# Kernel tuning notes

Hardware: AMD Instinct MI355X
Metric: run time of the kernel (lower is better)

The kernel has to match this reference:

```python
import jax, jax.numpy as jnp
import numpy as np

NPOINT = 512
NSAMPLE = 32
RADIUS = 0.2


def furthest_point_sampling(pts, npoint):
    # pts: (B, N, 3) -> (B, npoint) int32 indices
    B, N, _ = pts.shape

    def step(carry, _):
        dist, far = carry  # (B,N), (B,)
        centroid = jnp.take_along_axis(pts, far[:, None, None], axis=1)  # (B,1,3)
        d2 = jnp.sum((pts - centroid) ** 2, axis=-1)  # (B,N)
        dist = jnp.minimum(dist, d2)
        nfar = jnp.argmax(dist, axis=-1).astype(jnp.int32)
        return (dist, nfar), far

    init = (jnp.full((B, N), 1e10, pts.dtype), jnp.zeros((B,), jnp.int32))
    _, idxs = jax.lax.scan(step, init, None, length=npoint)
    return idxs.T  # (B, npoint)


def ball_query(new_xyz, xyz, nsample, radius):
    # new_xyz: (B,S,3), xyz: (B,N,3) -> (B,S,nsample) int32
    N = xyz.shape[1]
    d2 = jnp.sum((new_xyz[:, :, None, :] - xyz[:, None, :, :]) ** 2, axis=-1)  # (B,S,N)
    ar = jnp.arange(N, dtype=jnp.int32)
    key = jnp.where(d2 < radius * radius, ar, N)  # valid idx, else sentinel N
    idx = jnp.sort(key, axis=-1)[..., :nsample]  # first nsample in-radius indices
    first = idx[..., :1]
    idx = jnp.where(idx == N, first, idx)  # pad with first valid (CUDA ball_query behavior)
    return jnp.minimum(idx, N - 1)


def group_points(feat, idx):
    # feat: (B,C,N), idx: (B,S,K) -> (B,C,S,K)
    return jax.vmap(lambda f, i: f[:, i])(feat, idx)


def pointnet_sa(xyz, features, W1, b1, W2, b2, W3, b3):
    xyz_t = jnp.transpose(xyz, (0, 2, 1))  # (B,N,3)
    fps_idx = furthest_point_sampling(xyz_t, NPOINT)  # (B,S)
    new_xyz = group_points(xyz, fps_idx[:, :, None])[..., 0]  # (B,3,S)
    idx = ball_query(jnp.transpose(new_xyz, (0, 2, 1)), xyz_t, NSAMPLE, RADIUS)  # (B,S,K)
    grouped_xyz = group_points(xyz, idx) - new_xyz[:, :, :, None]  # (B,3,S,K), centered
    grouped_feat = group_points(features, idx)  # (B,C,S,K)
    h = jnp.concatenate([grouped_xyz, grouped_feat], axis=1)  # (B,C+3,S,K)
    for W, b in ((W1, b1), (W2, b2), (W3, b3)):
        h = jax.nn.relu(jnp.einsum('oc,bcsk->bosk', W, h) + b[None, :, None, None])
    new_features = jnp.max(h, axis=3)  # (B,out,S)
    return new_xyz, new_features


def setup_inputs() -> dict:
    key = jax.random.key(0)
    ks = jax.random.split(key, 8)
    B, N, C = 16, 2048, 64
    return {
        'xyz': jax.random.uniform(ks[0], (B, 3, N), dtype=jnp.float32),
        'features': jax.random.normal(ks[1], (B, C, N), dtype=jnp.float32),
        'W1': jax.random.normal(ks[2], (64, 67), dtype=jnp.float32) * 0.1,
        'b1': jnp.zeros((64,), jnp.float32),
        'W2': jax.random.normal(ks[3], (128, 64), dtype=jnp.float32) * 0.1,
        'b2': jnp.zeros((128,), jnp.float32),
        'W3': jax.random.normal(ks[4], (256, 128), dtype=jnp.float32) * 0.1,
        'b3': jnp.zeros((256,), jnp.float32),
    }


def reference(xyz, features, W1, b1, W2, b2, W3, b3):
    return pointnet_sa(xyz, features, W1, b1, W2, b2, W3, b3)
```

## Files before the change

kernel.cpp:

```cpp
#include <hip/hip_runtime.h>

#define NB 16
#define NN 2048
#define NP 512
#define NS 32
#define NC 64

typedef _Float16 f16x8 __attribute__((ext_vector_type(8)));
typedef _Float16 f16x4 __attribute__((ext_vector_type(4)));
typedef float f32x4 __attribute__((ext_vector_type(4)));
typedef float f32x2 __attribute__((ext_vector_type(2)));

__device__ __forceinline__ float sqdist(float dx, float dy, float dz) {
  return __fadd_rn(__fadd_rn(__fmul_rn(dx, dx), __fmul_rn(dy, dy)), __fmul_rn(dz, dz));
}

__device__ __forceinline__ f32x2 pk_add(f32x2 a, f32x2 b) {
  f32x2 d;
  asm("v_pk_add_f32 %0, %1, %2" : "=v"(d) : "v"(a), "v"(b));
  return d;
}
__device__ __forceinline__ f32x2 pk_mul(f32x2 a, f32x2 b) {
  f32x2 d;
  asm("v_pk_mul_f32 %0, %1, %2" : "=v"(d) : "v"(a), "v"(b));
  return d;
}

template <int CTRL>
__device__ __forceinline__ float dppmaxf(float m) {
  int t = __builtin_amdgcn_update_dpp(0, __float_as_int(m), CTRL, 0xf, 0xf, true);
  return fmaxf(m, __int_as_float(t));
}
template <int CTRL>
__device__ __forceinline__ unsigned dppmaxu(unsigned m) {
  int t = __builtin_amdgcn_update_dpp(0, (int)m, CTRL, 0xf, 0xf, true);
  return m > (unsigned)t ? m : (unsigned)t;
}

__global__ __launch_bounds__(256) void prep_kernel(const float* __restrict__ feat,
                                                   const float* __restrict__ xyz,
                                                   _Float16* __restrict__ featF,
                                                   float* __restrict__ xyzT) {
  __shared__ float tile[64][65];
  const int b = blockIdx.x;
  const int n0 = blockIdx.y * 64;
  const int t = threadIdx.x;
  const int g = t >> 6, l = t & 63;
  if (g == 0) {
    int n = n0 + l;
    float4 q;
    q.x = xyz[(size_t)b * 3 * NN + n];
    q.y = xyz[(size_t)b * 3 * NN + NN + n];
    q.z = xyz[(size_t)b * 3 * NN + 2 * NN + n];
    q.w = 0.f;
    ((float4*)xyzT)[(size_t)b * NN + n] = q;
  }
#pragma unroll
  for (int r = 0; r < 16; ++r) {
    int c = g * 16 + r;
    tile[c][l] = feat[((size_t)b * NC + c) * NN + n0 + l];
  }
  __syncthreads();
#pragma unroll
  for (int r = 0; r < 16; ++r) {
    int nl = g * 16 + r;
    featF[((size_t)(b * NN + n0 + nl)) * NC + l] = (_Float16)tile[l][nl];
  }
}

__global__ __launch_bounds__(256) void wconv_kernel(const float* __restrict__ W1,
                                                    const float* __restrict__ W2,
                                                    const float* __restrict__ W3,
                                                    _Float16* __restrict__ W1f,
                                                    _Float16* __restrict__ W2f,
                                                    _Float16* __restrict__ W3f) {
  int i = blockIdx.x * 256 + threadIdx.x;
  if (i < 64 * 96) {
    int o = i / 96, k = i - o * 96;
    float v = (k < 64) ? W1[o * 67 + 3 + k] : ((k < 67) ? W1[o * 67 + (k - 64)] : 0.f);
    W1f[i] = (_Float16)v;
  }
  if (i < 128 * 64) W2f[i] = (_Float16)W2[i];
  if (i < 256 * 128) W3f[i] = (_Float16)W3[i];
}

__global__ __launch_bounds__(128, 1) void fps_kernel(const float* __restrict__ xyz,
                                                     float* __restrict__ newxyz) {
  const int b = blockIdx.x, t = threadIdx.x;
  const int w = t >> 6;
  const float* X = xyz + (size_t)b * 3 * NN;
  __shared__ __align__(16) float4 XL[NN];
  __shared__ float cst[3][NP];
  __shared__ __align__(16) uint2 pairx[2][2];
  f32x2 px[8], py[8], pz[8], dist[8];
#pragma unroll
  for (int jj = 0; jj < 8; ++jj) {
    int n0 = t + 256 * jj, n1 = n0 + 128;
    px[jj] = f32x2{X[n0], X[n1]};
    py[jj] = f32x2{X[NN + n0], X[NN + n1]};
    pz[jj] = f32x2{X[2 * NN + n0], X[2 * NN + n1]};
    dist[jj] = f32x2{1e10f, 1e10f};
    XL[n0] = make_float4(px[jj].x, py[jj].x, pz[jj].x, 0.f);
    XL[n1] = make_float4(px[jj].y, py[jj].y, pz[jj].y, 0.f);
  }
  float cx = X[0], cy = X[NN], cz = X[2 * NN];
  const unsigned kb = 2047u - (unsigned)t;
  __syncthreads();
  int buf = 0;
  for (int i = 0; i < NP; ++i) {
    if (t == 0) {
      cst[0][i] = cx;
      cst[1][i] = cy;
      cst[2][i] = cz;
    }
    const f32x2 ncx = f32x2{-cx, -cx}, ncy = f32x2{-cy, -cy}, ncz = f32x2{-cz, -cz};
    float hm[8];
#pragma unroll
    for (int jj = 0; jj < 8; ++jj) {
      f32x2 dx = pk_add(px[jj], ncx);
      f32x2 dy = pk_add(py[jj], ncy);
      f32x2 dz = pk_add(pz[jj], ncz);
      f32x2 s = pk_add(pk_add(pk_mul(dx, dx), pk_mul(dy, dy)), pk_mul(dz, dz));
      f32x2 d = dist[jj];
      d.x = fminf(d.x, s.x);
      d.y = fminf(d.y, s.y);
      dist[jj] = d;
      hm[jj] = fmaxf(d.x, d.y);
    }
    float m = fmaxf(fmaxf(fmaxf(hm[0], hm[1]), fmaxf(hm[2], hm[3])),
                    fmaxf(fmaxf(hm[4], hm[5]), fmaxf(hm[6], hm[7])));
    m = dppmaxf<0x111>(m);
    m = dppmaxf<0x112>(m);
    m = dppmaxf<0x114>(m);
    m = dppmaxf<0x118>(m);
    m = dppmaxf<0x142>(m);
    m = dppmaxf<0x143>(m);
    const float vmax =
        __int_as_float(__builtin_amdgcn_readlane(__float_as_int(m), 63));
    unsigned jk = 0;
#pragma unroll
    for (int jj = 0; jj < 8; ++jj) {
      unsigned c0 = (dist[jj].x == vmax) ? (63u - 2u * jj) : 0u;
      unsigned c1 = (dist[jj].y == vmax) ? (63u - (2u * jj + 1u)) : 0u;
      unsigned c = c0 > c1 ? c0 : c1;
      jk = jk > c ? jk : c;
    }
    unsigned nk = (jk >= 48u) ? (kb - ((63u - jk) << 7)) : 0u;
    nk = dppmaxu<0x111>(nk);
    nk = dppmaxu<0x112>(nk);
    nk = dppmaxu<0x114>(nk);
    nk = dppmaxu<0x118>(nk);
    nk = dppmaxu<0x142>(nk);
    nk = dppmaxu<0x143>(nk);
    if ((t & 63) == 63) pairx[buf][w] = make_uint2(__float_as_uint(m), nk);
    __syncthreads();
    uint4 pr = *(const uint4*)&pairx[buf][0];
    bool take1 = (pr.z > pr.x) | ((pr.z == pr.x) & (pr.w > pr.y));
    unsigned ng = 2047u - (take1 ? pr.w : pr.y);
    float4 c = XL[ng];
    cx = c.x;
    cy = c.y;
    cz = c.z;
    buf ^= 1;
  }
  __syncthreads();
  for (int i = t; i < NP; i += 128) {
    newxyz[b * 3 * NP + i] = cst[0][i];
    newxyz[b * 3 * NP + NP + i] = cst[1][i];
    newxyz[b * 3 * NP + 2 * NP + i] = cst[2][i];
  }
}

__global__ __launch_bounds__(256) void ball_kernel(const float* __restrict__ xyz,
                                                   const float* __restrict__ newxyz,
                                                   int* __restrict__ idx) {
  const int b = blockIdx.x;
  const int s = blockIdx.y * 4 + (threadIdx.x >> 6);
  const int lane = threadIdx.x & 63;
  const float* X = xyz + (size_t)b * 3 * NN;
  const float cx = newxyz[b * 3 * NP + s];
  const float cy = newxyz[b * 3 * NP + NP + s];
  const float cz = newxyz[b * 3 * NP + 2 * NP + s];
  int* row = idx + ((size_t)(b * NP + s)) * NS;
  const float r2 = (float)(0.2 * 0.2);
  int total = 0, first = 0;
  bool havefirst = false;
  for (int c0 = 0; c0 < NN; c0 += 64) {
    int n = c0 + lane;
    float d2 = sqdist(X[n] - cx, X[NN + n] - cy, X[2 * NN + n] - cz);
    bool hit = d2 < r2;
    unsigned long long mask = __ballot(hit);
    if (!havefirst && mask) {
      first = c0 + __builtin_ctzll(mask);
      havefirst = true;
    }
    if (hit) {
      int pos = total + (int)__popcll(mask & ((1ull << lane) - 1ull));
      if (pos < NS) row[pos] = n;
    }
    total += (int)__popcll(mask);
    if (total >= NS) break;
  }
  if (total < NS && lane >= total && lane < NS) row[lane] = first;
}

#define HSTR 104
#define A1STR 72
#define A2STR 136
#define A1OFF 17408

__global__ __launch_bounds__(256) void mlp_kernel(
    const float* __restrict__ xyzT, const _Float16* __restrict__ featF,
    const int* __restrict__ idx, const float* __restrict__ newxyz,
    const _Float16* __restrict__ W1f, const float* __restrict__ b1,
    const _Float16* __restrict__ W2f, const float* __restrict__ b2,
    const _Float16* __restrict__ W3f, const float* __restrict__ b3, float* __restrict__ out) {
  __shared__ _Float16 smem[17408 + 9216];
  _Float16* hT = smem;
  _Float16* a1T = smem + A1OFF;
  const int b = blockIdx.x;
  const int s0 = blockIdx.y * 4;
  const int t = threadIdx.x;
  const int lane = t & 63, w = t >> 6;

  {
    const int col = t & 127, hf = t >> 7;
    const int s = s0 + (col >> 5), k = col & 31;
    const int n = idx[((size_t)(b * NP + s)) * NS + k];
    const _Float16* F = featF + (size_t)(b * NN + n) * NC;
#pragma unroll
    for (int j = 0; j < 4; ++j) {
      int p = hf * 4 + j;
      *(f16x8*)(&hT[col * HSTR + p * 8]) = *(const f16x8*)(F + p * 8);
    }
    if (hf == 0) {
      float4 pnt = ((const float4*)xyzT)[(size_t)b * NN + n];
      float cx = newxyz[b * 3 * NP + s];
      float cy = newxyz[b * 3 * NP + NP + s];
      float cz = newxyz[b * 3 * NP + 2 * NP + s];
      f16x8 v = {};
      v[0] = (_Float16)(pnt.x - cx);
      v[1] = (_Float16)(pnt.y - cy);
      v[2] = (_Float16)(pnt.z - cz);
      *(f16x8*)(&hT[col * HSTR + 64]) = v;
    } else {
      f16x8 z = {};
      *(f16x8*)(&hT[col * HSTR + 72]) = z;
      *(f16x8*)(&hT[col * HSTR + 80]) = z;
      *(f16x8*)(&hT[col * HSTR + 88]) = z;
    }
  }
  __syncthreads();

  const int cl = lane & 15;
  const int kg = lane >> 4;

  {
    f32x4 acc[8];
    {
      f32x4 bb = *(const f32x4*)(b1 + w * 16 + kg * 4);
#pragma unroll
      for (int ct = 0; ct < 8; ++ct) acc[ct] = bb;
    }
#pragma unroll
    for (int ks = 0; ks < 3; ++ks) {
      f16x8 A = *(const f16x8*)(W1f + (w * 16 + cl) * 96 + ks * 32 + kg * 8);
#pragma unroll
      for (int ct = 0; ct < 8; ++ct) {
        f16x8 B = *(const f16x8*)(&hT[(ct * 16 + cl) * HSTR + ks * 32 + kg * 8]);
        acc[ct] = __builtin_amdgcn_mfma_f32_16x16x32_f16(A, B, acc[ct], 0, 0, 0);
      }
    }
#pragma unroll
    for (int ct = 0; ct < 8; ++ct) {
      f16x4 v;
#pragma unroll
      for (int i2 = 0; i2 < 4; ++i2) v[i2] = (_Float16)fmaxf(acc[ct][i2], 0.f);
      *(f16x4*)(&a1T[(ct * 16 + cl) * A1STR + w * 16 + kg * 4]) = v;
    }
  }
  __syncthreads();

  {
    f32x4 acc[2][8];
#pragma unroll
    for (int r = 0; r < 2; ++r) {
      f32x4 bb = *(const f32x4*)(b2 + w * 32 + r * 16 + kg * 4);
#pragma unroll
      for (int ct = 0; ct < 8; ++ct) acc[r][ct] = bb;
    }
#pragma unroll
    for (int ks = 0; ks < 2; ++ks) {
      f16x8 A0 = *(const f16x8*)(W2f + (w * 32 + cl) * 64 + ks * 32 + kg * 8);
      f16x8 A1 = *(const f16x8*)(W2f + (w * 32 + 16 + cl) * 64 + ks * 32 + kg * 8);
#pragma unroll
      for (int ct = 0; ct < 8; ++ct) {
        f16x8 B = *(const f16x8*)(&a1T[(ct * 16 + cl) * A1STR + ks * 32 + kg * 8]);
        acc[0][ct] = __builtin_amdgcn_mfma_f32_16x16x32_f16(A0, B, acc[0][ct], 0, 0, 0);
        acc[1][ct] = __builtin_amdgcn_mfma_f32_16x16x32_f16(A1, B, acc[1][ct], 0, 0, 0);
      }
    }
#pragma unroll
    for (int r = 0; r < 2; ++r)
#pragma unroll
      for (int ct = 0; ct < 8; ++ct) {
        f16x4 v;
#pragma unroll
        for (int i2 = 0; i2 < 4; ++i2) v[i2] = (_Float16)fmaxf(acc[r][ct][i2], 0.f);
        *(f16x4*)(&hT[(ct * 16 + cl) * A2STR + w * 32 + r * 16 + kg * 4]) = v;
      }
  }
  __syncthreads();

  float* out2 = out + NB * 3 * NP;
#pragma unroll
  for (int rh = 0; rh < 2; ++rh) {
    f32x4 acc[2][8];
#pragma unroll
    for (int r = 0; r < 2; ++r) {
      f32x4 bb = *(const f32x4*)(b3 + w * 64 + rh * 32 + r * 16 + kg * 4);
#pragma unroll
      for (int ct = 0; ct < 8; ++ct) acc[r][ct] = bb;
    }
#pragma unroll
    for (int ks = 0; ks < 4; ++ks) {
      f16x8 A0 = *(const f16x8*)(W3f + (w * 64 + rh * 32 + cl) * 128 + ks * 32 + kg * 8);
      f16x8 A1 = *(const f16x8*)(W3f + (w * 64 + rh * 32 + 16 + cl) * 128 + ks * 32 + kg * 8);
#pragma unroll
      for (int ct = 0; ct < 8; ++ct) {
        f16x8 B = *(const f16x8*)(&hT[(ct * 16 + cl) * A2STR + ks * 32 + kg * 8]);
        acc[0][ct] = __builtin_amdgcn_mfma_f32_16x16x32_f16(A0, B, acc[0][ct], 0, 0, 0);
        acc[1][ct] = __builtin_amdgcn_mfma_f32_16x16x32_f16(A1, B, acc[1][ct], 0, 0, 0);
      }
    }
#pragma unroll
    for (int r = 0; r < 2; ++r)
#pragma unroll
      for (int sl = 0; sl < 4; ++sl) {
        float vv[4];
#pragma unroll
        for (int i2 = 0; i2 < 4; ++i2) {
          float m0 = fmaxf(acc[r][sl * 2][i2], 0.f);
          float m1 = fmaxf(acc[r][sl * 2 + 1][i2], 0.f);
          float mv = fmaxf(m0, m1);
          mv = fmaxf(mv, __shfl_xor(mv, 1, 64));
          mv = fmaxf(mv, __shfl_xor(mv, 2, 64));
          mv = fmaxf(mv, __shfl_xor(mv, 4, 64));
          mv = fmaxf(mv, __shfl_xor(mv, 8, 64));
          vv[i2] = mv;
        }
        if (cl == 0) {
          int ob = w * 64 + rh * 32 + r * 16 + kg * 4;
#pragma unroll
          for (int i2 = 0; i2 < 4; ++i2)
            out2[((size_t)(b * 256 + ob + i2)) * NP + s0 + sl] = vv[i2];
        }
      }
  }
}

extern "C" void kernel_launch(void* const* d_in, const int* in_sizes, int n_in, void* d_out,
                              int out_size, void* d_ws, size_t ws_size, hipStream_t stream) {
  const float* xyz = (const float*)d_in[0];
  const float* feat = (const float*)d_in[1];
  const float* W1 = (const float*)d_in[2];
  const float* b1 = (const float*)d_in[3];
  const float* W2 = (const float*)d_in[4];
  const float* b2 = (const float*)d_in[5];
  const float* W3 = (const float*)d_in[6];
  const float* b3 = (const float*)d_in[7];
  float* out = (float*)d_out;
  char* ws = (char*)d_ws;
  float* xyzT = (float*)ws;
  _Float16* featF = (_Float16*)(ws + 524288);
  int* idx = (int*)(ws + 4718592);
  _Float16* W1f = (_Float16*)(ws + 5767168);
  _Float16* W2f = (_Float16*)(ws + 5779456);
  _Float16* W3f = (_Float16*)(ws + 5795840);

  hipLaunchKernelGGL(prep_kernel, dim3(NB, 32), dim3(256), 0, stream, feat, xyz, featF, xyzT);
  hipLaunchKernelGGL(wconv_kernel, dim3(128), dim3(256), 0, stream, W1, W2, W3, W1f, W2f, W3f);
  hipLaunchKernelGGL(fps_kernel, dim3(NB), dim3(128), 0, stream, xyz, out);
  hipLaunchKernelGGL(ball_kernel, dim3(NB, 128), dim3(256), 0, stream, xyz, out, idx);
  hipLaunchKernelGGL(mlp_kernel, dim3(NB, 128), dim3(256), 0, stream, xyzT, featF, idx, out, W1f,
                     b1, W2f, b2, W3f, b3, out);
}
```

Baseline: 395.9 us.

## Merge prep, weight-convert and FPS into one kernel; widen FPS to 256 threads

Folds the feature transpose/convert, weight conversion and furthest point sampling into a single launch. Blocks 0-15 run FPS, blocks 16-527 do the prep tiles, and block 528 converts the weights, so the prep work overlaps the serial FPS. FPS now uses 256 threads with 8 points per thread instead of 16. The argmax-index search uses ballot plus count-trailing-zeros instead of a second DPP reduction. The trade-off is a 4-way cross-wave combine per iteration in place of 2-way, and the shared-memory footprint is shared with the prep path.

```diff
diff --git a/kernel.cpp b/kernel.cpp
--- a/kernel.cpp
+++ b/kernel.cpp
@@ -31,71 +31,68 @@
   int t = __builtin_amdgcn_update_dpp(0, __float_as_int(m), CTRL, 0xf, 0xf, true);
   return fmaxf(m, __int_as_float(t));
 }
-template <int CTRL>
-__device__ __forceinline__ unsigned dppmaxu(unsigned m) {
-  int t = __builtin_amdgcn_update_dpp(0, (int)m, CTRL, 0xf, 0xf, true);
-  return m > (unsigned)t ? m : (unsigned)t;
-}
-
-__global__ __launch_bounds__(256) void prep_kernel(const float* __restrict__ feat,
-                                                   const float* __restrict__ xyz,
-                                                   _Float16* __restrict__ featF,
-                                                   float* __restrict__ xyzT) {
-  __shared__ float tile[64][65];
-  const int b = blockIdx.x;
-  const int n0 = blockIdx.y * 64;
+
+__global__ __launch_bounds__(256, 1) void front_kernel(
+    const float* __restrict__ xyz, const float* __restrict__ feat,
+    const float* __restrict__ W1, const float* __restrict__ W2, const float* __restrict__ W3,
+    float* __restrict__ newxyz, _Float16* __restrict__ featF, float* __restrict__ xyzT,
+    _Float16* __restrict__ W1f, _Float16* __restrict__ W2f, _Float16* __restrict__ W3f) {
+  __shared__ __align__(16) char sm[39040];
+  const int bid = blockIdx.x;
   const int t = threadIdx.x;
-  const int g = t >> 6, l = t & 63;
-  if (g == 0) {
-    int n = n0 + l;
-    float4 q;
-    q.x = xyz[(size_t)b * 3 * NN + n];
-    q.y = xyz[(size_t)b * 3 * NN + NN + n];
-    q.z = xyz[(size_t)b * 3 * NN + 2 * NN + n];
-    q.w = 0.f;
-    ((float4*)xyzT)[(size_t)b * NN + n] = q;
-  }
-#pragma unroll
-  for (int r = 0; r < 16; ++r) {
-    int c = g * 16 + r;
-    tile[c][l] = feat[((size_t)b * NC + c) * NN + n0 + l];
-  }
-  __syncthreads();
-#pragma unroll
-  for (int r = 0; r < 16; ++r) {
-    int nl = g * 16 + r;
-    featF[((size_t)(b * NN + n0 + nl)) * NC + l] = (_Float16)tile[l][nl];
-  }
-}
-
-__global__ __launch_bounds__(256) void wconv_kernel(const float* __restrict__ W1,
-                                                    const float* __restrict__ W2,
-                                                    const float* __restrict__ W3,
-                                                    _Float16* __restrict__ W1f,
-                                                    _Float16* __restrict__ W2f,
-                                                    _Float16* __restrict__ W3f) {
-  int i = blockIdx.x * 256 + threadIdx.x;
-  if (i < 64 * 96) {
-    int o = i / 96, k = i - o * 96;
-    float v = (k < 64) ? W1[o * 67 + 3 + k] : ((k < 67) ? W1[o * 67 + (k - 64)] : 0.f);
-    W1f[i] = (_Float16)v;
-  }
-  if (i < 128 * 64) W2f[i] = (_Float16)W2[i];
-  if (i < 256 * 128) W3f[i] = (_Float16)W3[i];
-}
-
-__global__ __launch_bounds__(128, 1) void fps_kernel(const float* __restrict__ xyz,
-                                                     float* __restrict__ newxyz) {
-  const int b = blockIdx.x, t = threadIdx.x;
+
+  if (bid >= 16) {
+    if (bid == 528) {
+      for (int i = t; i < 256 * 128; i += 256) {
+        if (i < 64 * 96) {
+          int o = i / 96, k = i - o * 96;
+          float v = (k < 64) ? W1[o * 67 + 3 + k] : ((k < 67) ? W1[o * 67 + (k - 64)] : 0.f);
+          W1f[i] = (_Float16)v;
+        }
+        if (i < 128 * 64) W2f[i] = (_Float16)W2[i];
+        W3f[i] = (_Float16)W3[i];
+      }
+      return;
+    }
+    float(*tile)[65] = (float(*)[65])sm;
+    const int pb = bid - 16;
+    const int b = pb >> 5;
+    const int n0 = (pb & 31) * 64;
+    const int g = t >> 6, l = t & 63;
+    if (g == 0) {
+      int n = n0 + l;
+      float4 q;
+      q.x = xyz[(size_t)b * 3 * NN + n];
+      q.y = xyz[(size_t)b * 3 * NN + NN + n];
+      q.z = xyz[(size_t)b * 3 * NN + 2 * NN + n];
+      q.w = 0.f;
+      ((float4*)xyzT)[(size_t)b * NN + n] = q;
+    }
+#pragma unroll
+    for (int r = 0; r < 16; ++r) {
+      int c = g * 16 + r;
+      tile[c][l] = feat[((size_t)b * NC + c) * NN + n0 + l];
+    }
+    __syncthreads();
+#pragma unroll
+    for (int r = 0; r < 16; ++r) {
+      int nl = g * 16 + r;
+      featF[((size_t)(b * NN + n0 + nl)) * NC + l] = (_Float16)tile[l][nl];
+    }
+    return;
+  }
+
+  const int b = bid;
   const int w = t >> 6;
   const float* X = xyz + (size_t)b * 3 * NN;
-  __shared__ __align__(16) float4 XL[NN];
-  __shared__ float cst[3][NP];
-  __shared__ __align__(16) uint2 pairx[2][2];
-  f32x2 px[8], py[8], pz[8], dist[8];
-#pragma unroll
-  for (int jj = 0; jj < 8; ++jj) {
-    int n0 = t + 256 * jj, n1 = n0 + 128;
+  float4* XL = (float4*)sm;
+  float* cst = (float*)(sm + 32768);
+  uint2* ck = (uint2*)(sm + 32768 + 6144);
+
+  f32x2 px[4], py[4], pz[4], dist[4];
+#pragma unroll
+  for (int jj = 0; jj < 4; ++jj) {
+    int n0 = t + 256 * jj, n1 = n0 + 1024;
     px[jj] = f32x2{X[n0], X[n1]};
     py[jj] = f32x2{X[NN + n0], X[NN + n1]};
     pz[jj] = f32x2{X[2 * NN + n0], X[2 * NN + n1]};
@@ -104,19 +101,18 @@
     XL[n1] = make_float4(px[jj].y, py[jj].y, pz[jj].y, 0.f);
   }
   float cx = X[0], cy = X[NN], cz = X[2 * NN];
-  const unsigned kb = 2047u - (unsigned)t;
   __syncthreads();
   int buf = 0;
   for (int i = 0; i < NP; ++i) {
     if (t == 0) {
-      cst[0][i] = cx;
-      cst[1][i] = cy;
-      cst[2][i] = cz;
+      cst[i] = cx;
+      cst[NP + i] = cy;
+      cst[2 * NP + i] = cz;
     }
     const f32x2 ncx = f32x2{-cx, -cx}, ncy = f32x2{-cy, -cy}, ncz = f32x2{-cz, -cz};
-    float hm[8];
-#pragma unroll
-    for (int jj = 0; jj < 8; ++jj) {
+    float hm[4];
+#pragma unroll
+    for (int jj = 0; jj < 4; ++jj) {
       f32x2 dx = pk_add(px[jj], ncx);
       f32x2 dy = pk_add(py[jj], ncy);
       f32x2 dz = pk_add(pz[jj], ncz);
@@ -127,47 +123,43 @@
       dist[jj] = d;
       hm[jj] = fmaxf(d.x, d.y);
     }
-    float m = fmaxf(fmaxf(fmaxf(hm[0], hm[1]), fmaxf(hm[2], hm[3])),
-                    fmaxf(fmaxf(hm[4], hm[5]), fmaxf(hm[6], hm[7])));
+    float m = fmaxf(fmaxf(hm[0], hm[1]), fmaxf(hm[2], hm[3]));
     m = dppmaxf<0x111>(m);
     m = dppmaxf<0x112>(m);
     m = dppmaxf<0x114>(m);
     m = dppmaxf<0x118>(m);
     m = dppmaxf<0x142>(m);
     m = dppmaxf<0x143>(m);
-    const float vmax =
-        __int_as_float(__builtin_amdgcn_readlane(__float_as_int(m), 63));
-    unsigned jk = 0;
-#pragma unroll
-    for (int jj = 0; jj < 8; ++jj) {
-      unsigned c0 = (dist[jj].x == vmax) ? (63u - 2u * jj) : 0u;
-      unsigned c1 = (dist[jj].y == vmax) ? (63u - (2u * jj + 1u)) : 0u;
-      unsigned c = c0 > c1 ? c0 : c1;
-      jk = jk > c ? jk : c;
-    }
-    unsigned nk = (jk >= 48u) ? (kb - ((63u - jk) << 7)) : 0u;
-    nk = dppmaxu<0x111>(nk);
-    nk = dppmaxu<0x112>(nk);
-    nk = dppmaxu<0x114>(nk);
-    nk = dppmaxu<0x118>(nk);
-    nk = dppmaxu<0x142>(nk);
-    nk = dppmaxu<0x143>(nk);
-    if ((t & 63) == 63) pairx[buf][w] = make_uint2(__float_as_uint(m), nk);
+    const float vmax = __int_as_float(__builtin_amdgcn_readlane(__float_as_int(m), 63));
+    unsigned long long mm[8];
+#pragma unroll
+    for (int jj = 0; jj < 4; ++jj) {
+      mm[jj] = __ballot(dist[jj].x == vmax);
+      mm[4 + jj] = __ballot(dist[jj].y == vmax);
+    }
+    unsigned nw = 0;
+#pragma unroll
+    for (int q = 7; q >= 0; --q)
+      if (mm[q]) nw = 256u * (unsigned)q + (unsigned)(w << 6) + (unsigned)__builtin_ctzll(mm[q]);
+    if ((t & 63) == 0) ck[buf * 4 + w] = make_uint2(__float_as_uint(vmax), nw);
     __syncthreads();
-    uint4 pr = *(const uint4*)&pairx[buf][0];
-    bool take1 = (pr.z > pr.x) | ((pr.z == pr.x) & (pr.w > pr.y));
-    unsigned ng = 2047u - (take1 ? pr.w : pr.y);
-    float4 c = XL[ng];
+    uint4 c01 = *(const uint4*)&ck[buf * 4 + 0];
+    uint4 c23 = *(const uint4*)&ck[buf * 4 + 2];
+    unsigned v = c01.x, n = c01.y;
+    if (c01.z > v || (c01.z == v && c01.w < n)) { v = c01.z; n = c01.w; }
+    if (c23.x > v || (c23.x == v && c23.y < n)) { v = c23.x; n = c23.y; }
+    if (c23.z > v || (c23.z == v && c23.w < n)) { v = c23.z; n = c23.w; }
+    float4 c = XL[n];
     cx = c.x;
     cy = c.y;
     cz = c.z;
     buf ^= 1;
   }
   __syncthreads();
-  for (int i = t; i < NP; i += 128) {
-    newxyz[b * 3 * NP + i] = cst[0][i];
-    newxyz[b * 3 * NP + NP + i] = cst[1][i];
-    newxyz[b * 3 * NP + 2 * NP + i] = cst[2][i];
+  for (int i = t; i < NP; i += 256) {
+    newxyz[b * 3 * NP + i] = cst[i];
+    newxyz[b * 3 * NP + NP + i] = cst[NP + i];
+    newxyz[b * 3 * NP + 2 * NP + i] = cst[2 * NP + i];
   }
 }
 
@@ -378,9 +370,8 @@
   _Float16* W2f = (_Float16*)(ws + 5779456);
   _Float16* W3f = (_Float16*)(ws + 5795840);
 
-  hipLaunchKernelGGL(prep_kernel, dim3(NB, 32), dim3(256), 0, stream, feat, xyz, featF, xyzT);
-  hipLaunchKernelGGL(wconv_kernel, dim3(128), dim3(256), 0, stream, W1, W2, W3, W1f, W2f, W3f);
-  hipLaunchKernelGGL(fps_kernel, dim3(NB), dim3(128), 0, stream, xyz, out);
+  hipLaunchKernelGGL(front_kernel, dim3(529), dim3(256), 0, stream, xyz, feat, W1, W2, W3, out,
+                     featF, xyzT, W1f, W2f, W3f);
   hipLaunchKernelGGL(ball_kernel, dim3(NB, 128), dim3(256), 0, stream, xyz, out, idx);
   hipLaunchKernelGGL(mlp_kernel, dim3(NB, 128), dim3(256), 0, stream, xyzT, featF, idx, out, W1f,
                      b1, W2f, b2, W3f, b3, out);
```

Measured after the change: 378.0 us. 4.5% less time.
